# Kernel tuning notes

Hardware: AMD Instinct MI355X
Metric: run time of the kernel (lower is better)

## Reference

```python
import jax, jax.numpy as jnp
import numpy as np

N, E, H, C, G = 100000, 400000, 4, 64, 64  # nodes, edges, heads, per-head dim, graphs
NEG_SLOPE = 0.2


def gat_conv(x, src, dst, W, a_src, a_dst, b, num_nodes):
    # PyG GATConv (v1), concat=True, eval mode (no dropout).
    h = (x @ W).reshape(num_nodes, H, C)                      # [N,H,C]
    al_src = (h * a_src).sum(-1)                              # [N,H]
    al_dst = (h * a_dst).sum(-1)                              # [N,H]
    e = jax.nn.leaky_relu(al_src[src] + al_dst[dst], NEG_SLOPE)  # [E',H]
    # segment softmax over incoming edges of each destination node
    m = jax.ops.segment_max(e, dst, num_segments=num_nodes)
    m = jnp.where(jnp.isfinite(m), m, 0.0)
    ex = jnp.exp(e - m[dst])
    s = jax.ops.segment_sum(ex, dst, num_segments=num_nodes)
    alpha = ex / (s[dst] + 1e-16)                             # [E',H]
    msg = h[src] * alpha[..., None]                           # [E',H,C]
    out = jax.ops.segment_sum(msg, dst, num_segments=num_nodes)
    return out.reshape(num_nodes, H * C) + b


def setup_inputs() -> dict:
    key = jax.random.key(0)
    ks = jax.random.split(key, 20)
    p = lambda k, shape: (jax.random.normal(k, shape, dtype=jnp.float32) * 0.05)
    inp = {
        "x": jax.random.normal(ks[0], (N, 2), dtype=jnp.float32),
        "edge_index": jax.random.randint(ks[1], (2, E), 0, N, dtype=jnp.int64),
        "batch": jnp.sort(jax.random.randint(ks[2], (N,), 0, G, dtype=jnp.int64)),
        # layer 1: in=2 -> heads*hidden=256
        "W1": p(ks[3], (2, H * C)), "a1s": p(ks[4], (H, C)), "a1d": p(ks[5], (H, C)), "b1": jnp.zeros((H * C,), jnp.float32),
        # layer 2,3: 256 -> 256
        "W2": p(ks[6], (H * C, H * C)), "a2s": p(ks[7], (H, C)), "a2d": p(ks[8], (H, C)), "b2": jnp.zeros((H * C,), jnp.float32),
        "W3": p(ks[9], (H * C, H * C)), "a3s": p(ks[10], (H, C)), "a3d": p(ks[11], (H, C)), "b3": jnp.zeros((H * C,), jnp.float32),
        # projection MLP 256 -> 512 -> 256
        "Wp1": p(ks[12], (H * C, 512)), "bp1": jnp.zeros((512,), jnp.float32),
        "Wp2": p(ks[13], (512, 256)), "bp2": jnp.zeros((256,), jnp.float32),
    }
    return inp


def reference(x, edge_index, batch, W1, a1s, a1d, b1, W2, a2s, a2d, b2,
              W3, a3s, a3d, b3, Wp1, bp1, Wp2, bp2):
    num_nodes = x.shape[0]
    # add_self_loops=True (PyG GATConv default); same edge set for all layers
    loops = jnp.arange(num_nodes, dtype=edge_index.dtype)
    src = jnp.concatenate([edge_index[0], loops])
    dst = jnp.concatenate([edge_index[1], loops])

    h = jax.nn.elu(gat_conv(x, src, dst, W1, a1s, a1d, b1, num_nodes))
    h = jax.nn.elu(gat_conv(h, src, dst, W2, a2s, a2d, b2, num_nodes))
    h = jax.nn.elu(gat_conv(h, src, dst, W3, a3s, a3d, b3, num_nodes))

    # global_mean_pool over graphs
    sums = jax.ops.segment_sum(h, batch, num_segments=G)            # [G,256]
    cnts = jax.ops.segment_sum(jnp.ones((num_nodes,), h.dtype), batch, num_segments=G)
    pooled = sums / jnp.maximum(cnts, 1.0)[:, None]

    # projection MLP (dropout is identity in eval)
    z = jax.nn.relu(pooled @ Wp1 + bp1)
    return z @ Wp2 + bp2
```

## Files before the change

kernel.cpp:

```cpp
#include <hip/hip_runtime.h>
#include <math.h>

#define HC 256
#define NHEAD 4
#define NEG_SLOPE 0.2f
#define GG 64

typedef unsigned short u16;
typedef unsigned int u32;
typedef __attribute__((ext_vector_type(8))) short short8;
typedef __attribute__((ext_vector_type(4))) float f32x4;

static __device__ inline u16 f2bf_rn(float f) {
  u32 x = __float_as_uint(f);
  u32 r = (x + 0x7fffu + ((x >> 16) & 1u)) >> 16;
  return (u16)r;
}
static __device__ inline float bf2f(u16 u) { return __uint_as_float(((u32)u) << 16); }
static __device__ inline int swz(int b) { return b ^ (((b >> 8) & 7) << 4); }


__global__ void count_deg_kernel(const int* __restrict__ ei, int E, int Nn, int* __restrict__ deg) {
  int idx = blockIdx.x * 256 + threadIdx.x;
  int Et = E + Nn;
  if (idx >= Et) return;
  int d = (idx < E) ? ei[E + idx] : (idx - E);
  atomicAdd(&deg[d], 1);
}

__global__ void scan_partial_kernel(const int* __restrict__ deg, int Nn,
                                    int* __restrict__ rowptr, int* __restrict__ bsum) {
  __shared__ int s[256];
  int t = threadIdx.x, i = blockIdx.x * 256 + t;
  int v = (i < Nn) ? deg[i] : 0;
  s[t] = v; __syncthreads();
  for (int off = 1; off < 256; off <<= 1) {
    int x = (t >= off) ? s[t - off] : 0; __syncthreads();
    s[t] += x; __syncthreads();
  }
  if (i < Nn) rowptr[i] = s[t] - v;
  if (t == 255) bsum[blockIdx.x] = s[t];
}

__global__ void scan_bsum_kernel(int* __restrict__ bsum, int nb) {
  __shared__ int s[512];
  int t = threadIdx.x;
  int v = (t < nb) ? bsum[t] : 0;
  s[t] = v; __syncthreads();
  for (int off = 1; off < 512; off <<= 1) {
    int x = (t >= off) ? s[t - off] : 0; __syncthreads();
    s[t] += x; __syncthreads();
  }
  if (t < nb) bsum[t] = s[t] - v;
}

__global__ void scan_add_kernel(int* __restrict__ rowptr, const int* __restrict__ bsum,
                                int Nn, int Etot) {
  int i = blockIdx.x * 256 + threadIdx.x;
  if (i < Nn) rowptr[i] += bsum[blockIdx.x];
  if (i == 0) rowptr[Nn] = Etot;
}

__global__ void fill_csr_kernel(const int* __restrict__ ei, int E, int Nn,
                                const int* __restrict__ rowptr, int* __restrict__ cursor,
                                int* __restrict__ col) {
  int idx = blockIdx.x * 256 + threadIdx.x;
  int Et = E + Nn;
  if (idx >= Et) return;
  int s, d;
  if (idx < E) { s = ei[idx]; d = ei[E + idx]; } else { s = d = idx - E; }
  int pos = atomicAdd(&cursor[d], 1);
  col[rowptr[d] + pos] = s;
}


__global__ void convert_w_kernel(const float* __restrict__ W, u16* __restrict__ hi) {
  int idx = blockIdx.x * 256 + threadIdx.x;
  if (idx >= 256 * 256) return;
  int k = idx >> 8, n = idx & 255;
  hi[n * 256 + k] = f2bf_rn(W[idx]);
}


__global__ void prep_va_kernel(const float* __restrict__ W1, const float* __restrict__ a1s,
                               const float* __restrict__ a1d, float* __restrict__ va) {
  int t = threadIdx.x;
  int q = t >> 6, lane = t & 63;
  int c = t;
  float asv = a1s[c], adv = a1d[c];
  float w0 = W1[c], w1 = W1[256 + c];
  float s0 = w0 * asv, s1 = w1 * asv, d0 = w0 * adv, d1 = w1 * adv;
  #pragma unroll
  for (int off = 32; off >= 1; off >>= 1) {
    s0 += __shfl_xor(s0, off, 64); s1 += __shfl_xor(s1, off, 64);
    d0 += __shfl_xor(d0, off, 64); d1 += __shfl_xor(d1, off, 64);
  }
  if (lane == 0) {
    va[q] = s0; va[4 + q] = s1;
    va[8 + q] = d0; va[12 + q] = d1;
  }
}

__global__ void logits1_kernel(const float* __restrict__ x, const float* __restrict__ va,
                               float* __restrict__ als, float* __restrict__ ald, int Nn) {
  int node = blockIdx.x * 256 + threadIdx.x;
  if (node >= Nn) return;
  float2 xv = *(const float2*)&x[(size_t)node * 2];
  float4 vs0 = *(const float4*)&va[0], vs1 = *(const float4*)&va[4];
  float4 vd0 = *(const float4*)&va[8], vd1 = *(const float4*)&va[12];
  float4 s, d;
  s.x = xv.x * vs0.x + xv.y * vs1.x; s.y = xv.x * vs0.y + xv.y * vs1.y;
  s.z = xv.x * vs0.z + xv.y * vs1.z; s.w = xv.x * vs0.w + xv.y * vs1.w;
  d.x = xv.x * vd0.x + xv.y * vd1.x; d.y = xv.x * vd0.y + xv.y * vd1.y;
  d.z = xv.x * vd0.z + xv.y * vd1.z; d.w = xv.x * vd0.w + xv.y * vd1.w;
  *(float4*)&als[node * 4] = s;
  *(float4*)&ald[node * 4] = d;
}

__global__ void sm_gather1_kernel(const float* __restrict__ x,
    const float* __restrict__ als, const float* __restrict__ ald,
    const int* __restrict__ rowptr, const int* __restrict__ col,
    float* __restrict__ xbar, int Nn) {
  int node = blockIdx.x * 256 + threadIdx.x;
  if (node >= Nn) return;
  int rs = rowptr[node], re = rowptr[node + 1];
  float4 ad = *(const float4*)&ald[node * 4];
  float S0 = 0.f, S1 = 0.f, S2 = 0.f, S3 = 0.f;
  float a0 = 0.f, a1 = 0.f, a2 = 0.f, a3 = 0.f, a4 = 0.f, a5 = 0.f, a6 = 0.f, a7 = 0.f;
  for (int i = rs; i < re; ++i) {
    int s = col[i];
    float4 a = *(const float4*)&als[(size_t)s * 4];
    float2 xs = *(const float2*)&x[(size_t)s * 2];
    float e0 = a.x + ad.x; e0 = e0 > 0.f ? e0 : NEG_SLOPE * e0;
    float e1 = a.y + ad.y; e1 = e1 > 0.f ? e1 : NEG_SLOPE * e1;
    float e2 = a.z + ad.z; e2 = e2 > 0.f ? e2 : NEG_SLOPE * e2;
    float e3 = a.w + ad.w; e3 = e3 > 0.f ? e3 : NEG_SLOPE * e3;
    float p0 = __expf(e0), p1 = __expf(e1), p2 = __expf(e2), p3 = __expf(e3);
    S0 += p0; S1 += p1; S2 += p2; S3 += p3;
    a0 += p0 * xs.x; a1 += p0 * xs.y;
    a2 += p1 * xs.x; a3 += p1 * xs.y;
    a4 += p2 * xs.x; a5 += p2 * xs.y;
    a6 += p3 * xs.x; a7 += p3 * xs.y;
  }
  float i0 = 1.f / (S0 + 1e-16f), i1 = 1.f / (S1 + 1e-16f);
  float i2 = 1.f / (S2 + 1e-16f), i3 = 1.f / (S3 + 1e-16f);
  *(float4*)&xbar[(size_t)node * 8]     = make_float4(a0 * i0, a1 * i0, a2 * i1, a3 * i1);
  *(float4*)&xbar[(size_t)node * 8 + 4] = make_float4(a4 * i2, a5 * i2, a6 * i3, a7 * i3);
}

__global__ __launch_bounds__(256) void expand1_kernel(const float* __restrict__ xbar,
    const float* __restrict__ W1, const float* __restrict__ b1,
    u16* __restrict__ out16, int Nn) {
  int node = blockIdx.x * 4 + (threadIdx.x >> 6);
  int lane = threadIdx.x & 63;
  if (node >= Nn) return;
  int hA = lane >> 5;
  float4 xb0 = *(const float4*)&xbar[(size_t)node * 8];
  float4 xb1 = *(const float4*)&xbar[(size_t)node * 8 + 4];
  float xA0 = hA ? xb0.z : xb0.x, xA1 = hA ? xb0.w : xb0.y;
  float xB0 = hA ? xb1.z : xb1.x, xB1 = hA ? xb1.w : xb1.y;
  int cA = 2 * lane, cB = 128 + 2 * lane;
  float2 wA0 = *(const float2*)&W1[cA], wA1 = *(const float2*)&W1[256 + cA];
  float2 wB0 = *(const float2*)&W1[cB], wB1 = *(const float2*)&W1[256 + cB];
  float2 bA = *(const float2*)&b1[cA],  bB = *(const float2*)&b1[cB];
  float o0 = xA0 * wA0.x + xA1 * wA1.x + bA.x;
  float o1 = xA0 * wA0.y + xA1 * wA1.y + bA.y;
  float o2 = xB0 * wB0.x + xB1 * wB1.x + bB.x;
  float o3 = xB0 * wB0.y + xB1 * wB1.y + bB.y;
  o0 = o0 > 0.f ? o0 : (__expf(o0) - 1.0f);
  o1 = o1 > 0.f ? o1 : (__expf(o1) - 1.0f);
  o2 = o2 > 0.f ? o2 : (__expf(o2) - 1.0f);
  o3 = o3 > 0.f ? o3 : (__expf(o3) - 1.0f);
  u32* o32 = (u32*)out16;
  o32[(size_t)node * 128 + lane]      = (u32)f2bf_rn(o0) | ((u32)f2bf_rn(o1) << 16);
  o32[(size_t)node * 128 + 64 + lane] = (u32)f2bf_rn(o2) | ((u32)f2bf_rn(o3) << 16);
}


#define GBM 128
#define GBN 128

__global__ __launch_bounds__(256) void gemm_mfma_kernel(
    const u16* __restrict__ A, const u16* __restrict__ Bt,
    const float* __restrict__ as_, const float* __restrict__ ad_,
    u16* __restrict__ C16, float* __restrict__ als, float* __restrict__ ald, int Mrows) {
  __shared__ __align__(16) u16 sA[2][4096];
  __shared__ __align__(16) u16 sB[2][4096];
  char* sAc = (char*)&sA[0][0];
  char* sBc = (char*)&sB[0][0];
  int bc = blockIdx.x, br = blockIdx.y;
  int tid = threadIdx.x;
  int wid = tid >> 6, lane = tid & 63;
  int wr = wid >> 1, wc = wid & 1;
  int row0 = br * GBM, col0 = bc * GBN;
  int fr = lane & 15, fg = lane >> 4;

  const u16* agp[2];
  const u16* bgp[2];
  int wof[2];
  #pragma unroll
  for (int j = 0; j < 2; ++j) {
    int rr = wid * 32 + j * 16 + (lane >> 2);
    int kc = lane & 3;
    int gr = row0 + rr; if (gr >= Mrows) gr = Mrows - 1;
    agp[j] = A + (size_t)gr * 256 + kc * 8;
    bgp[j] = Bt + (size_t)(col0 + rr) * 256 + kc * 8;
    wof[j] = swz(rr * 64 + kc * 16);
  }
  int rofA[4], rofB[4];
  #pragma unroll
  for (int m = 0; m < 4; ++m) rofA[m] = swz((wr * 64 + m * 16 + fr) * 64 + fg * 16);
  #pragma unroll
  for (int n = 0; n < 4; ++n) rofB[n] = swz((wc * 64 + n * 16 + fr) * 64 + fg * 16);

  f32x4 acc[4][4];
  #pragma unroll
  for (int m = 0; m < 4; ++m)
    #pragma unroll
    for (int n = 0; n < 4; ++n) acc[m][n] = (f32x4){0.f, 0.f, 0.f, 0.f};

  uint4 va[2], vb[2];
  #pragma unroll
  for (int j = 0; j < 2; ++j) { va[j] = *(const uint4*)agp[j]; vb[j] = *(const uint4*)bgp[j]; }
  #pragma unroll
  for (int j = 0; j < 2; ++j) {
    *(uint4*)(sAc + wof[j]) = va[j];
    *(uint4*)(sBc + wof[j]) = vb[j];
  }
  __syncthreads();

  #pragma unroll
  for (int kt = 0; kt < 8; ++kt) {
    int buf = kt & 1;
    if (kt < 7) {
      #pragma unroll
      for (int j = 0; j < 2; ++j) {
        va[j] = *(const uint4*)(agp[j] + (kt + 1) * 32);
        vb[j] = *(const uint4*)(bgp[j] + (kt + 1) * 32);
      }
    }
    short8 af[4], bf[4];
    #pragma unroll
    for (int m = 0; m < 4; ++m) af[m] = *(const short8*)(sAc + buf * 8192 + rofA[m]);
    #pragma unroll
    for (int n = 0; n < 4; ++n) bf[n] = *(const short8*)(sBc + buf * 8192 + rofB[n]);
    #pragma unroll
    for (int m = 0; m < 4; ++m)
      #pragma unroll
      for (int n = 0; n < 4; ++n)
        acc[m][n] = __builtin_amdgcn_mfma_f32_16x16x32_bf16(af[m], bf[n], acc[m][n], 0, 0, 0);
    if (kt < 7) {
      int nb = buf ^ 1;
      #pragma unroll
      for (int j = 0; j < 2; ++j) {
        *(uint4*)(sAc + nb * 8192 + wof[j]) = va[j];
        *(uint4*)(sBc + nb * 8192 + wof[j]) = vb[j];
      }
      __syncthreads();
    }
  }

  #pragma unroll
  for (int m = 0; m < 4; ++m) {
    #pragma unroll
    for (int n = 0; n < 4; ++n) {
      int col = col0 + wc * 64 + n * 16 + fr;
      #pragma unroll
      for (int j = 0; j < 4; ++j) {
        int row = row0 + wr * 64 + m * 16 + fg * 4 + j;
        if (row < Mrows) C16[(size_t)row * 256 + col] = f2bf_rn(acc[m][n][j]);
      }
    }
  }

  int head = bc * 2 + wc;
  float asv[4], adv[4];
  #pragma unroll
  for (int n = 0; n < 4; ++n) {
    asv[n] = as_[head * 64 + n * 16 + fr];
    adv[n] = ad_[head * 64 + n * 16 + fr];
  }
  #pragma unroll
  for (int m = 0; m < 4; ++m) {
    #pragma unroll
    for (int j = 0; j < 4; ++j) {
      float ps = 0.f, pd = 0.f;
      #pragma unroll
      for (int n = 0; n < 4; ++n) {
        ps += acc[m][n][j] * asv[n];
        pd += acc[m][n][j] * adv[n];
      }
      #pragma unroll
      for (int off = 1; off < 16; off <<= 1) {
        ps += __shfl_xor(ps, off, 64);
        pd += __shfl_xor(pd, off, 64);
      }
      int grow = row0 + wr * 64 + m * 16 + fg * 4 + j;
      if (fr == 0 && grow < Mrows) {
        als[grow * 4 + head] = ps;
        ald[grow * 4 + head] = pd;
      }
    }
  }
}


__global__ void edge_softmax_kernel(const float* __restrict__ als, const float* __restrict__ ald,
                                    const int* __restrict__ rowptr, const int* __restrict__ col,
                                    float* __restrict__ w, float* __restrict__ invS, int Nn) {
  int node = blockIdx.x * 256 + threadIdx.x;
  if (node >= Nn) return;
  int rs = rowptr[node], re = rowptr[node + 1];
  float4 ad = *(const float4*)&ald[node * 4];
  float S0 = 0.f, S1 = 0.f, S2 = 0.f, S3 = 0.f;
  for (int i = rs; i < re; ++i) {
    int s = col[i];
    float4 a = *(const float4*)&als[(size_t)s * 4];
    float e0 = a.x + ad.x; e0 = e0 > 0.f ? e0 : NEG_SLOPE * e0;
    float e1 = a.y + ad.y; e1 = e1 > 0.f ? e1 : NEG_SLOPE * e1;
    float e2 = a.z + ad.z; e2 = e2 > 0.f ? e2 : NEG_SLOPE * e2;
    float e3 = a.w + ad.w; e3 = e3 > 0.f ? e3 : NEG_SLOPE * e3;
    float p0 = __expf(e0), p1 = __expf(e1), p2 = __expf(e2), p3 = __expf(e3);
    *(float4*)&w[(size_t)i * 4] = make_float4(p0, p1, p2, p3);
    S0 += p0; S1 += p1; S2 += p2; S3 += p3;
  }
  *(float4*)&invS[node * 4] = make_float4(1.f / (S0 + 1e-16f), 1.f / (S1 + 1e-16f),
                                          1.f / (S2 + 1e-16f), 1.f / (S3 + 1e-16f));
}


__global__ __launch_bounds__(256) void gat_gather_kernel(const u16* __restrict__ h16,
    const float* __restrict__ w, const float* __restrict__ invS,
    const int* __restrict__ rowptr, const int* __restrict__ col,
    const float* __restrict__ bias, u16* __restrict__ out16, int Nn) {
  int node = __builtin_amdgcn_readfirstlane(blockIdx.x * 4 + (threadIdx.x >> 6));
  int lane = threadIdx.x & 63;
  if (node >= Nn) return;
  int rs = rowptr[node], re = rowptr[node + 1];
  int head = lane >> 4;
  float a0 = 0.f, a1 = 0.f, a2 = 0.f, a3 = 0.f;
  const uint2* h64 = (const uint2*)h16;
  #pragma unroll 2
  for (int i = rs; i < re; ++i) {
    int s = col[i];
    float wq = w[(size_t)i * 4 + head];
    uint2 p = h64[(size_t)s * 64 + lane];
    a0 += wq * __uint_as_float(p.x << 16);
    a1 += wq * __uint_as_float(p.x & 0xffff0000u);
    a2 += wq * __uint_as_float(p.y << 16);
    a3 += wq * __uint_as_float(p.y & 0xffff0000u);
  }
  float iS = invS[node * 4 + head];
  float4 bv = *(const float4*)&bias[4 * lane];
  float o0 = a0 * iS + bv.x;
  float o1 = a1 * iS + bv.y;
  float o2 = a2 * iS + bv.z;
  float o3 = a3 * iS + bv.w;
  o0 = o0 > 0.f ? o0 : (__expf(o0) - 1.0f);
  o1 = o1 > 0.f ? o1 : (__expf(o1) - 1.0f);
  o2 = o2 > 0.f ? o2 : (__expf(o2) - 1.0f);
  o3 = o3 > 0.f ? o3 : (__expf(o3) - 1.0f);
  uint2 ov;
  ov.x = (u32)f2bf_rn(o0) | ((u32)f2bf_rn(o1) << 16);
  ov.y = (u32)f2bf_rn(o2) | ((u32)f2bf_rn(o3) << 16);
  ((uint2*)out16)[(size_t)node * 64 + lane] = ov;
}


__global__ void bounds_kernel(const int* __restrict__ batch, int Nn, int* __restrict__ bounds) {
  int g = threadIdx.x;
  if (g > GG) return;
  int lo = 0, hi = Nn;
  while (lo < hi) { int mid = (lo + hi) >> 1; if (batch[mid] < g) lo = mid + 1; else hi = mid; }
  bounds[g] = lo;
}

__global__ __launch_bounds__(64) void pool_kernel(const u16* __restrict__ X,
    const int* __restrict__ bounds, float* __restrict__ pooled) {
  int g = blockIdx.x, split = blockIdx.y;
  int lane = threadIdx.x;
  int s = bounds[g], e = bounds[g + 1];
  int cnt = e - s;
  if (cnt <= 0) return;
  int chunk = (cnt + gridDim.y - 1) / gridDim.y;
  int s2 = s + split * chunk, e2 = min(e, s2 + chunk);
  if (s2 >= e2) return;
  int r = lane >> 5, c = lane & 31;
  float acc[8] = {};
  for (int n = s2 + r; n < e2; n += 2) {
    uint4 v = *(const uint4*)&X[(size_t)n * HC + c * 8];
    acc[0] += __uint_as_float(v.x << 16);
    acc[1] += __uint_as_float(v.x & 0xffff0000u);
    acc[2] += __uint_as_float(v.y << 16);
    acc[3] += __uint_as_float(v.y & 0xffff0000u);
    acc[4] += __uint_as_float(v.z << 16);
    acc[5] += __uint_as_float(v.z & 0xffff0000u);
    acc[6] += __uint_as_float(v.w << 16);
    acc[7] += __uint_as_float(v.w & 0xffff0000u);
  }
  #pragma unroll
  for (int j = 0; j < 8; ++j) acc[j] += __shfl_xor(acc[j], 32, 64);
  if (r == 0) {
    #pragma unroll
    for (int j = 0; j < 8; ++j) atomicAdd(&pooled[g * HC + c * 8 + j], acc[j]);
  }
}

__global__ __launch_bounds__(512) void mlp_kernel(const float* __restrict__ pooled,
    const int* __restrict__ bounds, const float* __restrict__ Wp1, const float* __restrict__ bp1,
    const float* __restrict__ Wp2, const float* __restrict__ bp2, float* __restrict__ out) {
  __shared__ float p[256];
  __shared__ float z1[512];
  int g = blockIdx.x, t = threadIdx.x;
  if (t < 256) {
    int cnt = bounds[g + 1] - bounds[g];
    float inv = 1.0f / (float)(cnt > 1 ? cnt : 1);
    p[t] = pooled[g * 256 + t] * inv;
  }
  __syncthreads();
  float a1 = bp1[t];
  for (int k = 0; k < 256; ++k) a1 += p[k] * Wp1[k * 512 + t];
  z1[t] = fmaxf(a1, 0.f);
  __syncthreads();
  if (t < 256) {
    float a2 = bp2[t];
    for (int k = 0; k < 512; ++k) a2 += z1[k] * Wp2[k * 256 + t];
    out[g * 256 + t] = a2;
  }
}


static inline size_t align_up(size_t x, size_t a) { return (x + a - 1) & ~(a - 1); }

extern "C" void kernel_launch(void* const* d_in, const int* in_sizes, int n_in,
                              void* d_out, int out_size, void* d_ws, size_t ws_size,
                              hipStream_t stream) {
  const float* x    = (const float*)d_in[0];
  const int*   ei   = (const int*)d_in[1];
  const int*   batch= (const int*)d_in[2];
  const float* W1   = (const float*)d_in[3];
  const float* a1s  = (const float*)d_in[4];
  const float* a1d  = (const float*)d_in[5];
  const float* b1   = (const float*)d_in[6];
  const float* W2   = (const float*)d_in[7];
  const float* a2s  = (const float*)d_in[8];
  const float* a2d  = (const float*)d_in[9];
  const float* b2   = (const float*)d_in[10];
  const float* W3   = (const float*)d_in[11];
  const float* a3s  = (const float*)d_in[12];
  const float* a3d  = (const float*)d_in[13];
  const float* b3   = (const float*)d_in[14];
  const float* Wp1  = (const float*)d_in[15];
  const float* bp1  = (const float*)d_in[16];
  const float* Wp2  = (const float*)d_in[17];
  const float* bp2  = (const float*)d_in[18];

  const int N = in_sizes[0] / 2;
  const int E = in_sizes[1] / 2;
  const int Et = E + N;

  char* base = (char*)d_ws;
  size_t off = 0;
  auto alloc = [&](size_t bytes) { size_t o = off; off = align_up(off + bytes, 256); return o; };
  u16*   h16    = (u16*)  (base + alloc((size_t)N * HC * 2));
  u16*   xhi    = (u16*)  (base + alloc((size_t)N * HC * 2));
  float* als    = (float*)(base + alloc((size_t)N * 4 * 4));
  float* ald    = (float*)(base + alloc((size_t)N * 4 * 4));
  float* invS   = (float*)(base + alloc((size_t)N * 4 * 4));
  float* xbar   = (float*)(base + alloc((size_t)N * 8 * 4));
  float* vabuf  = (float*)(base + alloc(16 * 4));
  int*   rowptr = (int*)  (base + alloc((size_t)(N + 1) * 4));
  int*   col    = (int*)  (base + alloc((size_t)Et * 4));
  float* w      = (float*)(base + alloc((size_t)Et * 4 * 4));
  int*   deg    = (int*)  (base + alloc((size_t)N * 4));
  int*   cursor = (int*)  (base + alloc((size_t)N * 4));
  int*   bsum   = (int*)  (base + alloc(512 * 4));
  int*   bounds = (int*)  (base + alloc((GG + 1) * 4));
  float* pooled = (float*)(base + alloc((size_t)GG * HC * 4));
  (void)ws_size; (void)n_in; (void)out_size;

  u16* W2t = (u16*)deg;
  u16* W3t = (u16*)cursor;

  hipMemsetAsync(deg, 0, (size_t)N * 4, stream);
  hipMemsetAsync(cursor, 0, (size_t)N * 4, stream);
  hipMemsetAsync(pooled, 0, (size_t)GG * HC * 4, stream);

  int ebk = (Et + 255) / 256;
  count_deg_kernel<<<ebk, 256, 0, stream>>>(ei, E, N, deg);
  int NT = (N + 255) / 256;
  scan_partial_kernel<<<NT, 256, 0, stream>>>(deg, N, rowptr, bsum);
  scan_bsum_kernel<<<1, 512, 0, stream>>>(bsum, NT);
  scan_add_kernel<<<NT, 256, 0, stream>>>(rowptr, bsum, N, Et);
  fill_csr_kernel<<<ebk, 256, 0, stream>>>(ei, E, N, rowptr, cursor, col);

  convert_w_kernel<<<256, 256, 0, stream>>>(W2, W2t);
  convert_w_kernel<<<256, 256, 0, stream>>>(W3, W3t);

  dim3 gemm_grid(HC / GBN, (N + GBM - 1) / GBM);
  int nodeblk = (N + 3) / 4;

  prep_va_kernel<<<1, 256, 0, stream>>>(W1, a1s, a1d, vabuf);
  logits1_kernel<<<NT, 256, 0, stream>>>(x, vabuf, als, ald, N);
  sm_gather1_kernel<<<NT, 256, 0, stream>>>(x, als, ald, rowptr, col, xbar, N);
  expand1_kernel<<<nodeblk, 256, 0, stream>>>(xbar, W1, b1, xhi, N);
  gemm_mfma_kernel<<<gemm_grid, 256, 0, stream>>>(xhi, W2t, a2s, a2d, h16, als, ald, N);
  edge_softmax_kernel<<<NT, 256, 0, stream>>>(als, ald, rowptr, col, w, invS, N);
  gat_gather_kernel<<<nodeblk, 256, 0, stream>>>(h16, w, invS, rowptr, col, b2, xhi, N);
  gemm_mfma_kernel<<<gemm_grid, 256, 0, stream>>>(xhi, W3t, a3s, a3d, h16, als, ald, N);
  edge_softmax_kernel<<<NT, 256, 0, stream>>>(als, ald, rowptr, col, w, invS, N);
  gat_gather_kernel<<<nodeblk, 256, 0, stream>>>(h16, w, invS, rowptr, col, b3, xhi, N);

  bounds_kernel<<<1, 128, 0, stream>>>(batch, N, bounds);
  pool_kernel<<<dim3(GG, 32), 64, 0, stream>>>(xhi, bounds, pooled);
  mlp_kernel<<<GG, 512, 0, stream>>>(pooled, bounds, Wp1, bp1, Wp2, bp2, (float*)d_out);
}
```

Before: 381.6 us.

## Use direct global-to-LDS loads with triple buffering in MFMA GEMM

The GEMM tile staging now uses global_load_lds to copy A and B tiles straight into shared memory instead of routing them through registers. Shared memory grows to three buffers, so loads run two K-steps ahead, with manual vmcnt waits and barriers between steps. The per-lane global addresses are derived from the swizzled LDS layout so each lane's linear LDS write lands in the swizzled position. This is meant to cut register pressure and VGPR round trips and to overlap memory with MFMA. It adds more LDS use, which may lower occupancy, and it depends on hand-written waitcnt values being correct.

```diff
diff --git a/kernel.cpp b/kernel.cpp
--- a/kernel.cpp
+++ b/kernel.cpp
@@ -10,6 +10,9 @@
 typedef unsigned int u32;
 typedef __attribute__((ext_vector_type(8))) short short8;
 typedef __attribute__((ext_vector_type(4))) float f32x4;
+
+typedef __attribute__((address_space(1))) const void as1_void;
+typedef __attribute__((address_space(3))) void as3_void;
 
 static __device__ inline u16 f2bf_rn(float f) {
   u32 x = __float_as_uint(f);
@@ -184,10 +187,8 @@
     const u16* __restrict__ A, const u16* __restrict__ Bt,
     const float* __restrict__ as_, const float* __restrict__ ad_,
     u16* __restrict__ C16, float* __restrict__ als, float* __restrict__ ald, int Mrows) {
-  __shared__ __align__(16) u16 sA[2][4096];
-  __shared__ __align__(16) u16 sB[2][4096];
-  char* sAc = (char*)&sA[0][0];
-  char* sBc = (char*)&sB[0][0];
+  __shared__ __align__(16) u16 sA[3][4096];
+  __shared__ __align__(16) u16 sB[3][4096];
   int bc = blockIdx.x, br = blockIdx.y;
   int tid = threadIdx.x;
   int wid = tid >> 6, lane = tid & 63;
@@ -195,18 +196,23 @@
   int row0 = br * GBM, col0 = bc * GBN;
   int fr = lane & 15, fg = lane >> 4;
 
-  const u16* agp[2];
-  const u16* bgp[2];
-  int wof[2];
+  const u16* ga[2];
+  const u16* gb[2];
+  u16* lA[2];
+  u16* lB[2];
   #pragma unroll
   for (int j = 0; j < 2; ++j) {
-    int rr = wid * 32 + j * 16 + (lane >> 2);
-    int kc = lane & 3;
-    int gr = row0 + rr; if (gr >= Mrows) gr = Mrows - 1;
-    agp[j] = A + (size_t)gr * 256 + kc * 8;
-    bgp[j] = Bt + (size_t)(col0 + rr) * 256 + kc * 8;
-    wof[j] = swz(rr * 64 + kc * 16);
-  }
+    int sbase = j * 256 + wid * 64;
+    int s = sbase + lane;
+    int b = swz(s * 16);
+    int row = b >> 6, inner = (b & 63) >> 1;
+    int gr = row0 + row; if (gr >= Mrows) gr = Mrows - 1;
+    ga[j] = A  + (size_t)gr * 256 + inner;
+    gb[j] = Bt + (size_t)(col0 + row) * 256 + inner;
+    lA[j] = &sA[0][0] + sbase * 8;
+    lB[j] = &sB[0][0] + sbase * 8;
+  }
+
   int rofA[4], rofB[4];
   #pragma unroll
   for (int m = 0; m < 4; ++m) rofA[m] = swz((wr * 64 + m * 16 + fr) * 64 + fg * 16);
@@ -219,26 +225,28 @@
     #pragma unroll
     for (int n = 0; n < 4; ++n) acc[m][n] = (f32x4){0.f, 0.f, 0.f, 0.f};
 
-  uint4 va[2], vb[2];
-  #pragma unroll
-  for (int j = 0; j < 2; ++j) { va[j] = *(const uint4*)agp[j]; vb[j] = *(const uint4*)bgp[j]; }
-  #pragma unroll
-  for (int j = 0; j < 2; ++j) {
-    *(uint4*)(sAc + wof[j]) = va[j];
-    *(uint4*)(sBc + wof[j]) = vb[j];
-  }
-  __syncthreads();
+  auto stage = [&](int buf, int kt) {
+    #pragma unroll
+    for (int j = 0; j < 2; ++j) {
+      __builtin_amdgcn_global_load_lds((as1_void*)(ga[j] + kt * 32),
+                                       (as3_void*)(lA[j] + buf * 4096), 16, 0, 0);
+      __builtin_amdgcn_global_load_lds((as1_void*)(gb[j] + kt * 32),
+                                       (as3_void*)(lB[j] + buf * 4096), 16, 0, 0);
+    }
+  };
+
+  stage(0, 0);
+  stage(1, 1);
+  asm volatile("s_waitcnt vmcnt(4)\ns_barrier" ::: "memory");
+  __builtin_amdgcn_sched_barrier(0);
+
+  const char* sAc = (const char*)&sA[0][0];
+  const char* sBc = (const char*)&sB[0][0];
 
   #pragma unroll
   for (int kt = 0; kt < 8; ++kt) {
-    int buf = kt & 1;
-    if (kt < 7) {
-      #pragma unroll
-      for (int j = 0; j < 2; ++j) {
-        va[j] = *(const uint4*)(agp[j] + (kt + 1) * 32);
-        vb[j] = *(const uint4*)(bgp[j] + (kt + 1) * 32);
-      }
-    }
+    int buf = kt % 3;
+    if (kt + 2 < 8) stage((kt + 2) % 3, kt + 2);
     short8 af[4], bf[4];
     #pragma unroll
     for (int m = 0; m < 4; ++m) af[m] = *(const short8*)(sAc + buf * 8192 + rofA[m]);
@@ -249,15 +257,12 @@
       #pragma unroll
       for (int n = 0; n < 4; ++n)
         acc[m][n] = __builtin_amdgcn_mfma_f32_16x16x32_bf16(af[m], bf[n], acc[m][n], 0, 0, 0);
-    if (kt < 7) {
-      int nb = buf ^ 1;
-      #pragma unroll
-      for (int j = 0; j < 2; ++j) {
-        *(uint4*)(sAc + nb * 8192 + wof[j]) = va[j];
-        *(uint4*)(sBc + nb * 8192 + wof[j]) = vb[j];
-      }
-      __syncthreads();
+    if (kt + 2 < 8) {
+      asm volatile("s_waitcnt vmcnt(4) lgkmcnt(0)\ns_barrier" ::: "memory");
+    } else if (kt < 7) {
+      asm volatile("s_waitcnt vmcnt(0) lgkmcnt(0)\ns_barrier" ::: "memory");
     }
+    __builtin_amdgcn_sched_barrier(0);
   }
 
   #pragma unroll
```

Result: no change. 386.5 us (+1.3%).
